# Kernel optimization log

Hardware: AMD Instinct MI355X
Metric: run time of the kernel (lower is better)

Reference implementation:

```python
import jax, jax.numpy as jnp
import numpy as np

EMBED_DIM = 1024
NUM_HEADS = 16
HEAD_DIM = EMBED_DIM // NUM_HEADS


def setup_inputs() -> dict:
    key = jax.random.key(0)
    k1, k2, k3, k4 = jax.random.split(key, 4)
    scale = 1.0 / np.sqrt(EMBED_DIM)
    x = jax.random.normal(k1, (2, 2048, EMBED_DIM), dtype=jnp.float32)
    Wqkv = jax.random.normal(k2, (3 * EMBED_DIM, EMBED_DIM), dtype=jnp.float32) * scale
    Wproj = jax.random.normal(k3, (EMBED_DIM, EMBED_DIM), dtype=jnp.float32) * scale
    bproj = jax.random.normal(k4, (EMBED_DIM,), dtype=jnp.float32) * 0.01
    return {"x": x, "Wqkv": Wqkv, "Wproj": Wproj, "bproj": bproj}


def reference(x, Wqkv, Wproj, bproj):
    B, T, D = x.shape
    # QKV projection (torch Linear: x @ W.T), no bias
    qkv = jnp.einsum('btd,ed->bte', x, Wqkv)              # [B, T, 3D]
    qkv = qkv.reshape(B, T, 3, NUM_HEADS, HEAD_DIM)
    qkv = jnp.transpose(qkv, (2, 0, 3, 1, 4))             # [3, B, H, T, hd]
    q, k, v = qkv[0], qkv[1], qkv[2]
    # scaled dot-product attention (full matrix, as in source)
    dots = jnp.einsum('bhqd,bhkd->bhqk', q, k) / jnp.sqrt(jnp.asarray(HEAD_DIM, x.dtype))
    attn = jax.nn.softmax(dots, axis=-1)
    out = jnp.einsum('bhqk,bhkd->bhqd', attn, v)          # [B, H, T, hd]
    out = jnp.transpose(out, (0, 2, 1, 3)).reshape(B, T, D)
    # output projection with bias
    return jnp.einsum('btd,ed->bte', out, Wproj) + bproj
```

## Files before the change

### kernel.cpp

```cpp
#include <hip/hip_runtime.h>

typedef __attribute__((ext_vector_type(8))) short bf16x8;
typedef __attribute__((ext_vector_type(4))) short bf16x4;
typedef __attribute__((ext_vector_type(4))) float f32x4;
typedef __attribute__((ext_vector_type(2))) unsigned int u32x2;

#define MFMA32(a, b, c) __builtin_amdgcn_mfma_f32_16x16x32_bf16((a), (b), (c), 0, 0, 0)
#define MFMA16K(a, b, c) __builtin_amdgcn_mfma_f32_16x16x16bf16_1k((a), (b), (c), 0, 0, 0)

__device__ __forceinline__ unsigned short f2bf(float f) {
    unsigned u = __builtin_bit_cast(unsigned, f);
    u = (u + 0x7fffu + ((u >> 16) & 1u)) >> 16;
    return (unsigned short)u;
}

__device__ __forceinline__ unsigned cvtpk(float lo, float hi) {
    unsigned r;
    asm("v_cvt_pk_bf16_f32 %0, %1, %2" : "=v"(r) : "v"(lo), "v"(hi));
    return r;
}

__device__ __forceinline__ void gll16(const void* g, void* l) {
    __builtin_amdgcn_global_load_lds((__attribute__((address_space(1))) void*)g,
                                     (__attribute__((address_space(3))) void*)l,
                                     16, 0, 0);
}

__global__ __launch_bounds__(256) void castk(const float* __restrict__ in,
                                             unsigned short* __restrict__ out, int n) {
    int stride = gridDim.x * blockDim.x;
    for (int i = blockIdx.x * blockDim.x + threadIdx.x; i * 4 < n; i += stride) {
        float4 v = ((const float4*)in)[i];
        ushort4 o;
        o.x = f2bf(v.x); o.y = f2bf(v.y); o.z = f2bf(v.z); o.w = f2bf(v.w);
        ((ushort4*)out)[i] = o;
    }
}

template <int EPI>
__global__ __launch_bounds__(256) void gemm_bt(const unsigned short* __restrict__ A,
                                               const unsigned short* __restrict__ B,
                                               int K,
                                               unsigned short* __restrict__ qbuf,
                                               unsigned short* __restrict__ kbuf,
                                               unsigned short* __restrict__ vtb,
                                               float* __restrict__ outF,
                                               const float* __restrict__ bias) {
    __shared__ __align__(16) unsigned short As[2][4096];
    __shared__ __align__(16) unsigned short Bs[2][4096];
    const int tid = threadIdx.x;
    const int w = tid >> 6, l = tid & 63;
    const int g = l >> 4, cc = l & 15;
    const int wr = w >> 1, wc = w & 1;

    const int nwg = gridDim.x * gridDim.y;
    const int lin = blockIdx.y * gridDim.x + blockIdx.x;
    const int swz = (lin & 7) * (nwg >> 3) + (lin >> 3);
    const int bx = swz % gridDim.x, by = swz / gridDim.x;
    const int m0 = by * 128, n0 = bx * 128;

    f32x4 acc[4][4];
#pragma unroll
    for (int i = 0; i < 4; ++i)
#pragma unroll
        for (int j = 0; j < 4; ++j) acc[i][j] = (f32x4){0.f, 0.f, 0.f, 0.f};

    const int srow = (l >> 2);
    const int skk = (l & 3) * 8;

#define GSTAGE(bb, k0)                                                          \
    do {                                                                        \
        _Pragma("unroll") for (int ch = 0; ch < 2; ++ch) {                      \
            int ci = ch * 4 + w;                                                \
            int row = ci * 16 + srow;                                           \
            gll16(A + (size_t)(m0 + row) * K + (k0) + skk, &As[bb][ci * 512]);  \
            gll16(B + (size_t)(n0 + row) * K + (k0) + skk, &Bs[bb][ci * 512]);  \
        }                                                                       \
    } while (0)

    GSTAGE(0, 0);
    asm volatile("s_waitcnt vmcnt(0)" ::: "memory");
    __syncthreads();

    const int nt = K >> 5;
    int cur = 0;
    for (int t = 0; t < nt; ++t) {
        if (t + 1 < nt) GSTAGE(cur ^ 1, (t + 1) * 32);
        bf16x8 af[4], bfr[4];
#pragma unroll
        for (int i = 0; i < 4; ++i) {
            af[i]  = *(const bf16x8*)&As[cur][(wr * 64 + i * 16 + cc) * 32 + g * 8];
            bfr[i] = *(const bf16x8*)&Bs[cur][(wc * 64 + i * 16 + cc) * 32 + g * 8];
        }
#pragma unroll
        for (int i = 0; i < 4; ++i)
#pragma unroll
            for (int j = 0; j < 4; ++j) acc[i][j] = MFMA32(af[i], bfr[j], acc[i][j]);
        asm volatile("s_waitcnt vmcnt(0)" ::: "memory");
        __syncthreads();
        cur ^= 1;
    }
#undef GSTAGE

    if (EPI == 0) {
        const int which = n0 >> 10;
#pragma unroll
        for (int jn = 0; jn < 4; ++jn) {
            int n = n0 + wc * 64 + jn * 16 + cc;
            int hn = n & 1023;
            int h = hn >> 6, d = hn & 63;
#pragma unroll
            for (int i = 0; i < 4; ++i) {
#pragma unroll
                for (int j = 0; j < 4; ++j) {
                    int m = m0 + wr * 64 + i * 16 + g * 4 + j;
                    int b = m >> 11, t = m & 2047;
                    int bh = b * 16 + h;
                    float v = acc[i][jn][j];
                    if (which == 0) {
                        qbuf[((size_t)bh * 2048 + t) * 64 + d] = f2bf(v * 0.1803368801f);
                    } else if (which == 1) {
                        kbuf[((size_t)bh * 2048 + t) * 64 + d] = f2bf(v);
                    } else {
                        vtb[((size_t)bh * 64 + d) * 2048 + t] = f2bf(v);
                    }
                }
            }
        }
    } else {
#pragma unroll
        for (int jn = 0; jn < 4; ++jn) {
            int n = n0 + wc * 64 + jn * 16 + cc;
            float bn = bias[n];
#pragma unroll
            for (int i = 0; i < 4; ++i) {
#pragma unroll
                for (int j = 0; j < 4; ++j) {
                    int m = m0 + wr * 64 + i * 16 + g * 4 + j;
                    outF[(size_t)m * 1024 + n] = acc[i][jn][j] + bn;
                }
            }
        }
    }
}

__global__ __launch_bounds__(256) void attn_kernel(const unsigned short* __restrict__ qb,
                                                   const unsigned short* __restrict__ kb,
                                                   const unsigned short* __restrict__ vtb,
                                                   unsigned short* __restrict__ ao) {
    __shared__ __align__(16) unsigned short smem[16384];
    const int bh = blockIdx.y;
    const int w = threadIdx.x >> 6, l = threadIdx.x & 63;
    const int g = l >> 4, cc = l & 15;
    const int q0 = blockIdx.x * 128 + w * 32;

    const unsigned short* qbase = qb + (size_t)bh * 2048 * 64;
    const unsigned short* kbase = kb + (size_t)bh * 2048 * 64;
    const unsigned short* vbase = vtb + (size_t)bh * 64 * 2048;

    const int sl8 = l >> 3, sl7 = l & 7;
    const int sperm = ((sl7 ^ sl8) * 8);

#define STAGE(bb, kk)                                                                        \
    do {                                                                                     \
        int base = (bb) * 8192;                                                              \
        gll16(kbase + (size_t)((kk) + w * 8 + sl8) * 64 + sperm, &smem[base + w * 512]);     \
        gll16(kbase + (size_t)((kk) + (w + 4) * 8 + sl8) * 64 + sperm,                       \
              &smem[base + (w + 4) * 512]);                                                  \
        gll16(vbase + (size_t)(w * 8 + sl8) * 2048 + (kk) + sperm,                           \
              &smem[base + 4096 + w * 512]);                                                 \
        gll16(vbase + (size_t)((w + 4) * 8 + sl8) * 2048 + (kk) + sperm,                     \
              &smem[base + 4096 + (w + 4) * 512]);                                           \
    } while (0)

    bf16x8 qf[2][2];
#pragma unroll
    for (int qt = 0; qt < 2; ++qt)
#pragma unroll
        for (int kh = 0; kh < 2; ++kh)
            qf[qt][kh] = *(const bf16x8*)(qbase + (size_t)(q0 + qt * 16 + cc) * 64 + kh * 32 + g * 8);

    float mrun[2] = {-INFINITY, -INFINITY};
    float lrun[2] = {0.f, 0.f};
    f32x4 acc[2][4];
#pragma unroll
    for (int qt = 0; qt < 2; ++qt)
#pragma unroll
        for (int dt = 0; dt < 4; ++dt) acc[qt][dt] = (f32x4){0.f, 0.f, 0.f, 0.f};

    const int swz = cc & 7;

    STAGE(0, 0);
    asm volatile("s_waitcnt vmcnt(0)" ::: "memory");
    __syncthreads();

    for (int t = 0; t < 32; ++t) {
        const int cb = t & 1;
        if (t + 1 < 32) STAGE(cb ^ 1, (t + 1) * 64);

        const unsigned short* Kb = &smem[cb * 8192];
        const unsigned short* Vb = &smem[cb * 8192 + 4096];

        bf16x8 kf[4][2];
#pragma unroll
        for (int kt = 0; kt < 4; ++kt)
#pragma unroll
            for (int kh = 0; kh < 2; ++kh)
                kf[kt][kh] = *(const bf16x8*)&Kb[(kt * 16 + cc) * 64 + (((kh * 4 + g) ^ swz) * 8)];

        f32x4 s[2][4];
        __builtin_amdgcn_s_setprio(1);
#pragma unroll
        for (int qt = 0; qt < 2; ++qt)
#pragma unroll
            for (int kt = 0; kt < 4; ++kt) {
                f32x4 z = (f32x4){0.f, 0.f, 0.f, 0.f};
                z = MFMA32(kf[kt][0], qf[qt][0], z);
                z = MFMA32(kf[kt][1], qf[qt][1], z);
                s[qt][kt] = z;
            }
        __builtin_amdgcn_s_setprio(0);

        bf16x4 pf[2][4];
#pragma unroll
        for (int qt = 0; qt < 2; ++qt) {
            float mc = s[qt][0][0];
#pragma unroll
            for (int kt = 0; kt < 4; ++kt)
#pragma unroll
                for (int j = 0; j < 4; ++j) mc = fmaxf(mc, s[qt][kt][j]);
            mc = fmaxf(mc, __shfl_xor(mc, 16));
            mc = fmaxf(mc, __shfl_xor(mc, 32));
            float mnew = fmaxf(mrun[qt], mc);
            float fsc = __builtin_amdgcn_exp2f(mrun[qt] - mnew);
            mrun[qt] = mnew;
            float sum = 0.f;
#pragma unroll
            for (int kt = 0; kt < 4; ++kt)
#pragma unroll
                for (int j = 0; j < 4; ++j) {
                    float pv = __builtin_amdgcn_exp2f(s[qt][kt][j] - mnew);
                    s[qt][kt][j] = pv;
                    sum += pv;
                }
            lrun[qt] = lrun[qt] * fsc + sum;
#pragma unroll
            for (int dt = 0; dt < 4; ++dt) acc[qt][dt] = acc[qt][dt] * fsc;
#pragma unroll
            for (int kt = 0; kt < 4; ++kt) {
                u32x2 wv;
                wv.x = cvtpk(s[qt][kt][0], s[qt][kt][1]);
                wv.y = cvtpk(s[qt][kt][2], s[qt][kt][3]);
                pf[qt][kt] = __builtin_bit_cast(bf16x4, wv);
            }
        }

        __builtin_amdgcn_s_setprio(1);
#pragma unroll
        for (int kt = 0; kt < 4; ++kt) {
            const int seg = ((kt * 2 + (g >> 1)) ^ swz);
#pragma unroll
            for (int dt = 0; dt < 4; ++dt) {
                bf16x4 vf = *(const bf16x4*)&Vb[(dt * 16 + cc) * 64 + seg * 8 + (g & 1) * 4];
                acc[0][dt] = MFMA16K(vf, pf[0][kt], acc[0][dt]);
                acc[1][dt] = MFMA16K(vf, pf[1][kt], acc[1][dt]);
            }
        }
        __builtin_amdgcn_s_setprio(0);

        asm volatile("s_waitcnt vmcnt(0)" ::: "memory");
        __syncthreads();
    }
#undef STAGE

    const int b = bh >> 4, h = bh & 15;
#pragma unroll
    for (int qt = 0; qt < 2; ++qt) {
        float lsum = lrun[qt];
        lsum += __shfl_xor(lsum, 16);
        lsum += __shfl_xor(lsum, 32);
        float inv = 1.f / lsum;
        size_t rowbase = ((size_t)(b * 2048 + q0 + qt * 16 + cc)) * 1024 + h * 64;
#pragma unroll
        for (int dt = 0; dt < 4; ++dt) {
            u32x2 ov;
            ov.x = cvtpk(acc[qt][dt][0] * inv, acc[qt][dt][1] * inv);
            ov.y = cvtpk(acc[qt][dt][2] * inv, acc[qt][dt][3] * inv);
            *(u32x2*)(ao + rowbase + dt * 16 + g * 4) = ov;
        }
    }
}

extern "C" void kernel_launch(void* const* d_in, const int* in_sizes, int n_in,
                              void* d_out, int out_size, void* d_ws, size_t ws_size,
                              hipStream_t stream) {
    const float* x = (const float*)d_in[0];
    const float* Wqkv = (const float*)d_in[1];
    const float* Wproj = (const float*)d_in[2];
    const float* bproj = (const float*)d_in[3];
    float* out = (float*)d_out;

    unsigned short* xb = (unsigned short*)d_ws;
    unsigned short* wqkvb = xb + 4096 * 1024;
    unsigned short* wprojb = wqkvb + 3072 * 1024;
    unsigned short* qbuf = wprojb + 1024 * 1024;
    unsigned short* kbuf = qbuf + 32 * 2048 * 64;
    unsigned short* vtb = kbuf + 32 * 2048 * 64;
    unsigned short* aob = vtb + 32 * 2048 * 64;

    castk<<<1024, 256, 0, stream>>>(x, xb, 4096 * 1024);
    castk<<<1024, 256, 0, stream>>>(Wqkv, wqkvb, 3072 * 1024);
    castk<<<512, 256, 0, stream>>>(Wproj, wprojb, 1024 * 1024);

    gemm_bt<0><<<dim3(24, 32), 256, 0, stream>>>(xb, wqkvb, 1024, qbuf, kbuf, vtb, nullptr, nullptr);
    attn_kernel<<<dim3(16, 32), 256, 0, stream>>>(qbuf, kbuf, vtb, aob);
    gemm_bt<1><<<dim3(8, 32), 256, 0, stream>>>(aob, wprojb, 1024, nullptr, nullptr, nullptr, out, bproj);
}
```

Measured before the change: 212.0 us.

## Fuse cast kernels, narrow output-projection tiles, add lazy softmax rescaling

Merges the three fp32-to-bf16 cast launches into one kernel that indexes across all three buffers, removing two launches. The output-projection GEMM gets a 128x64 tile variant so it launches 512 workgroups instead of 256, which fills more CUs. MFMA priority hints are added around the GEMM inner loop. The attention softmax now rescales the accumulators only when some lane's new max exceeds the running max by more than a threshold; this saves exp and multiply work but lets bf16 probabilities grow up to about 2^11.5 before a rescale.

```diff
diff --git a/kernel.cpp b/kernel.cpp
--- a/kernel.cpp
+++ b/kernel.cpp
@@ -26,18 +26,29 @@
                                      16, 0, 0);
 }
 
-__global__ __launch_bounds__(256) void castk(const float* __restrict__ in,
-                                             unsigned short* __restrict__ out, int n) {
+__global__ __launch_bounds__(256) void castall(const float* __restrict__ x,
+                                               const float* __restrict__ wqkv,
+                                               const float* __restrict__ wproj,
+                                               unsigned short* __restrict__ xb,
+                                               unsigned short* __restrict__ wqkvb,
+                                               unsigned short* __restrict__ wprojb) {
+    const int N0 = 1048576, N1 = 786432, N2 = 262144;
     int stride = gridDim.x * blockDim.x;
-    for (int i = blockIdx.x * blockDim.x + threadIdx.x; i * 4 < n; i += stride) {
-        float4 v = ((const float4*)in)[i];
+    for (int i = blockIdx.x * blockDim.x + threadIdx.x; i < N0 + N1 + N2; i += stride) {
+        const float4* s;
+        ushort4* d;
+        int k;
+        if (i < N0) { s = (const float4*)x; d = (ushort4*)xb; k = i; }
+        else if (i < N0 + N1) { s = (const float4*)wqkv; d = (ushort4*)wqkvb; k = i - N0; }
+        else { s = (const float4*)wproj; d = (ushort4*)wprojb; k = i - N0 - N1; }
+        float4 v = s[k];
         ushort4 o;
         o.x = f2bf(v.x); o.y = f2bf(v.y); o.z = f2bf(v.z); o.w = f2bf(v.w);
-        ((ushort4*)out)[i] = o;
-    }
-}
-
-template <int EPI>
+        d[k] = o;
+    }
+}
+
+template <int EPI, int TN>
 __global__ __launch_bounds__(256) void gemm_bt(const unsigned short* __restrict__ A,
                                                const unsigned short* __restrict__ B,
                                                int K,
@@ -47,35 +58,46 @@
                                                float* __restrict__ outF,
                                                const float* __restrict__ bias) {
     __shared__ __align__(16) unsigned short As[2][4096];
-    __shared__ __align__(16) unsigned short Bs[2][4096];
+    __shared__ __align__(16) unsigned short Bs[2][TN * 32];
     const int tid = threadIdx.x;
     const int w = tid >> 6, l = tid & 63;
     const int g = l >> 4, cc = l & 15;
-    const int wr = w >> 1, wc = w & 1;
+    constexpr int MI = (TN == 128) ? 4 : 2;
+    const int wr = (TN == 128) ? (w >> 1) : w;
+    const int wc = (TN == 128) ? (w & 1) : 0;
 
     const int nwg = gridDim.x * gridDim.y;
     const int lin = blockIdx.y * gridDim.x + blockIdx.x;
     const int swz = (lin & 7) * (nwg >> 3) + (lin >> 3);
     const int bx = swz % gridDim.x, by = swz / gridDim.x;
-    const int m0 = by * 128, n0 = bx * 128;
-
-    f32x4 acc[4][4];
-#pragma unroll
-    for (int i = 0; i < 4; ++i)
+    const int m0 = by * 128, n0 = bx * TN;
+
+    f32x4 acc[MI][4];
+#pragma unroll
+    for (int i = 0; i < MI; ++i)
 #pragma unroll
         for (int j = 0; j < 4; ++j) acc[i][j] = (f32x4){0.f, 0.f, 0.f, 0.f};
 
     const int srow = (l >> 2);
     const int skk = (l & 3) * 8;
 
-#define GSTAGE(bb, k0)                                                          \
-    do {                                                                        \
-        _Pragma("unroll") for (int ch = 0; ch < 2; ++ch) {                      \
-            int ci = ch * 4 + w;                                                \
-            int row = ci * 16 + srow;                                           \
-            gll16(A + (size_t)(m0 + row) * K + (k0) + skk, &As[bb][ci * 512]);  \
-            gll16(B + (size_t)(n0 + row) * K + (k0) + skk, &Bs[bb][ci * 512]);  \
-        }                                                                       \
+#define GSTAGE(bb, k0)                                                              \
+    do {                                                                            \
+        _Pragma("unroll") for (int ch = 0; ch < 2; ++ch) {                          \
+            int ci = ch * 4 + w;                                                    \
+            gll16(A + (size_t)(m0 + ci * 16 + srow) * K + (k0) + skk,               \
+                  &As[bb][ci * 512]);                                               \
+        }                                                                           \
+        if constexpr (TN == 128) {                                                  \
+            _Pragma("unroll") for (int ch = 0; ch < 2; ++ch) {                      \
+                int ci = ch * 4 + w;                                                \
+                gll16(B + (size_t)(n0 + ci * 16 + srow) * K + (k0) + skk,           \
+                      &Bs[bb][ci * 512]);                                           \
+            }                                                                       \
+        } else {                                                                    \
+            gll16(B + (size_t)(n0 + w * 16 + srow) * K + (k0) + skk,                \
+                  &Bs[bb][w * 512]);                                                \
+        }                                                                           \
     } while (0)
 
     GSTAGE(0, 0);
@@ -86,16 +108,19 @@
     int cur = 0;
     for (int t = 0; t < nt; ++t) {
         if (t + 1 < nt) GSTAGE(cur ^ 1, (t + 1) * 32);
-        bf16x8 af[4], bfr[4];
-#pragma unroll
-        for (int i = 0; i < 4; ++i) {
-            af[i]  = *(const bf16x8*)&As[cur][(wr * 64 + i * 16 + cc) * 32 + g * 8];
-            bfr[i] = *(const bf16x8*)&Bs[cur][(wc * 64 + i * 16 + cc) * 32 + g * 8];
-        }
-#pragma unroll
-        for (int i = 0; i < 4; ++i)
+        bf16x8 af[MI], bfr[4];
+#pragma unroll
+        for (int i = 0; i < MI; ++i)
+            af[i] = *(const bf16x8*)&As[cur][(wr * (MI * 16) + i * 16 + cc) * 32 + g * 8];
+#pragma unroll
+        for (int j = 0; j < 4; ++j)
+            bfr[j] = *(const bf16x8*)&Bs[cur][(wc * 64 + j * 16 + cc) * 32 + g * 8];
+        __builtin_amdgcn_s_setprio(1);
+#pragma unroll
+        for (int i = 0; i < MI; ++i)
 #pragma unroll
             for (int j = 0; j < 4; ++j) acc[i][j] = MFMA32(af[i], bfr[j], acc[i][j]);
+        __builtin_amdgcn_s_setprio(0);
         asm volatile("s_waitcnt vmcnt(0)" ::: "memory");
         __syncthreads();
         cur ^= 1;
@@ -110,10 +135,10 @@
             int hn = n & 1023;
             int h = hn >> 6, d = hn & 63;
 #pragma unroll
-            for (int i = 0; i < 4; ++i) {
+            for (int i = 0; i < MI; ++i) {
 #pragma unroll
                 for (int j = 0; j < 4; ++j) {
-                    int m = m0 + wr * 64 + i * 16 + g * 4 + j;
+                    int m = m0 + wr * (MI * 16) + i * 16 + g * 4 + j;
                     int b = m >> 11, t = m & 2047;
                     int bh = b * 16 + h;
                     float v = acc[i][jn][j];
@@ -133,10 +158,10 @@
             int n = n0 + wc * 64 + jn * 16 + cc;
             float bn = bias[n];
 #pragma unroll
-            for (int i = 0; i < 4; ++i) {
+            for (int i = 0; i < MI; ++i) {
 #pragma unroll
                 for (int j = 0; j < 4; ++j) {
-                    int m = m0 + wr * 64 + i * 16 + g * 4 + j;
+                    int m = m0 + wr * (MI * 16) + i * 16 + g * 4 + j;
                     outF[(size_t)m * 1024 + n] = acc[i][jn][j] + bn;
                 }
             }
@@ -199,7 +224,7 @@
         if (t + 1 < 32) STAGE(cb ^ 1, (t + 1) * 64);
 
         const unsigned short* Kb = &smem[cb * 8192];
-        const unsigned short* Vb = &smem[cb * 8192 + 4096];
+        const unsigned short* Vb = Kb + 4096;
 
         bf16x8 kf[4][2];
 #pragma unroll
@@ -231,21 +256,24 @@
                 for (int j = 0; j < 4; ++j) mc = fmaxf(mc, s[qt][kt][j]);
             mc = fmaxf(mc, __shfl_xor(mc, 16));
             mc = fmaxf(mc, __shfl_xor(mc, 32));
-            float mnew = fmaxf(mrun[qt], mc);
-            float fsc = __builtin_amdgcn_exp2f(mrun[qt] - mnew);
-            mrun[qt] = mnew;
+            if (__any(mc > mrun[qt] + 11.5f)) {
+                float mnew = fmaxf(mrun[qt], mc);
+                float fsc = __builtin_amdgcn_exp2f(mrun[qt] - mnew);
+                mrun[qt] = mnew;
+                lrun[qt] *= fsc;
+#pragma unroll
+                for (int dt = 0; dt < 4; ++dt) acc[qt][dt] = acc[qt][dt] * fsc;
+            }
             float sum = 0.f;
 #pragma unroll
             for (int kt = 0; kt < 4; ++kt)
 #pragma unroll
                 for (int j = 0; j < 4; ++j) {
-                    float pv = __builtin_amdgcn_exp2f(s[qt][kt][j] - mnew);
+                    float pv = __builtin_amdgcn_exp2f(s[qt][kt][j] - mrun[qt]);
                     s[qt][kt][j] = pv;
                     sum += pv;
                 }
-            lrun[qt] = lrun[qt] * fsc + sum;
-#pragma unroll
-            for (int dt = 0; dt < 4; ++dt) acc[qt][dt] = acc[qt][dt] * fsc;
+            lrun[qt] += sum;
 #pragma unroll
             for (int kt = 0; kt < 4; ++kt) {
                 u32x2 wv;
@@ -308,11 +336,9 @@
     unsigned short* vtb = kbuf + 32 * 2048 * 64;
     unsigned short* aob = vtb + 32 * 2048 * 64;
 
-    castk<<<1024, 256, 0, stream>>>(x, xb, 4096 * 1024);
-    castk<<<1024, 256, 0, stream>>>(Wqkv, wqkvb, 3072 * 1024);
-    castk<<<512, 256, 0, stream>>>(Wproj, wprojb, 1024 * 1024);
-
-    gemm_bt<0><<<dim3(24, 32), 256, 0, stream>>>(xb, wqkvb, 1024, qbuf, kbuf, vtb, nullptr, nullptr);
+    castall<<<2048, 256, 0, stream>>>(x, Wqkv, Wproj, xb, wqkvb, wprojb);
+
+    gemm_bt<0, 128><<<dim3(24, 32), 256, 0, stream>>>(xb, wqkvb, 1024, qbuf, kbuf, vtb, nullptr, nullptr);
     attn_kernel<<<dim3(16, 32), 256, 0, stream>>>(qbuf, kbuf, vtb, aob);
-    gemm_bt<1><<<dim3(8, 32), 256, 0, stream>>>(aob, wprojb, 1024, nullptr, nullptr, nullptr, out, bproj);
-}
+    gemm_bt<1, 64><<<dim3(16, 32), 256, 0, stream>>>(aob, wprojb, 1024, nullptr, nullptr, nullptr, out, bproj);
+}
```

Result: faster. 202.2 us (-4.6%).
